# Optimization experiments

Measured on AMD Instinct MI355X. Metric: run time of the kernel, lower is better.

## Reference

```python
import jax, jax.numpy as jnp
import numpy as np

K = 8
LOCAL_WINDOW_RATIO = 0.25
NEG = -1e9
LN_EPS = 1e-5
NORM_EPS = 1e-12


def _window_indices(H, W):
    lws = max(3, int(min(H, W) * LOCAL_WINDOW_RATIO))
    if lws % 2 == 0:
        lws += 1
    half = lws // 2
    off = jnp.arange(-half, half + 1)
    dy, dx = jnp.meshgrid(off, off, indexing='ij')          # [lws,lws]
    dy = dy.reshape(-1); dx = dx.reshape(-1)                 # [w2]
    py, px = jnp.meshgrid(jnp.arange(H), jnp.arange(W), indexing='ij')
    py = py.reshape(-1); px = px.reshape(-1)                 # [HW]
    ny = py[:, None] + dy[None, :]                           # [HW,w2]
    nx = px[:, None] + dx[None, :]
    valid = (ny >= 0) & (ny < H) & (nx >= 0) & (nx < W)
    idx = jnp.clip(ny, 0, H - 1) * W + jnp.clip(nx, 0, W - 1)
    return idx, valid


def setup_inputs() -> dict:
    key = jax.random.key(0)
    ks = jax.random.split(key, 5)
    B, C, H, W = 4, 96, 48, 48
    return {
        'x': jax.random.normal(ks[0], (B, C, H, W), jnp.float32),
        'w1': jax.random.normal(ks[1], (2 * C, C), jnp.float32) * 0.05,
        'b1': jax.random.normal(ks[2], (2 * C,), jnp.float32) * 0.05,
        'w2': jax.random.normal(ks[3], (C, 2 * C), jnp.float32) * 0.05,
        'b2': jax.random.normal(ks[4], (C,), jnp.float32) * 0.05,
        'ln_w': jnp.ones((C,), jnp.float32),
        'ln_b': jnp.zeros((C,), jnp.float32),
    }


def reference(x, w1, b1, w2, b2, ln_w, ln_b):
    B, C, H, W = x.shape
    HW = H * W
    idx_w, valid = _window_indices(H, W)                     # [HW,w2]

    x_flat = x.transpose(0, 2, 3, 1).reshape(B, HW, C)       # [B,HW,C]
    n = jnp.linalg.norm(x_flat, axis=-1, keepdims=True)
    x_n = x_flat / jnp.maximum(n, NORM_EPS)

    win_n = x_n[:, idx_w, :]                                 # [B,HW,w2,C]
    sims = jnp.einsum('bpc,bpwc->bpw', x_n, win_n)           # cosine sim
    sims = jnp.where(valid[None], sims, NEG)

    # every pixel has >= (half+1)^2 >= K valid neighbors, so top-k stays valid
    top_sim, top_idx = jax.lax.top_k(sims, K)                # [B,HW,K]
    wts = jax.nn.softmax(top_sim, axis=-1)                   # exp/sum over top-k

    idx_g = jnp.take_along_axis(jnp.broadcast_to(idx_w[None], sims.shape), top_idx, axis=-1)  # [B,HW,K]
    feats = x_flat[jnp.arange(B)[:, None, None], idx_g]      # [B,HW,K,C] (un-normalized)
    agg = jnp.einsum('bpk,bpkc->bpc', wts, feats)            # [B,HW,C]

    mu = jnp.mean(x_flat, axis=-1, keepdims=True)
    var = jnp.var(x_flat, axis=-1, keepdims=True)
    x_ln = (x_flat - mu) / jnp.sqrt(var + LN_EPS) * ln_w + ln_b

    enhanced = agg + x_ln                                    # [B,HW,C]
    h = jax.nn.relu(jnp.einsum('bpc,dc->bpd', enhanced, w1) + b1)
    ffn = jnp.einsum('bpd,cd->bpc', h, w2) + b2
    out = enhanced + ffn
    return out.reshape(B, H, W, C).transpose(0, 3, 1, 2)
```

## Files before the change

### kernel.cpp

```cpp
#include <hip/hip_runtime.h>
#include <math.h>

#define BATCH 4
#define CH    96
#define HH    48
#define WW    48
#define HWPIX (HH*WW)
#define NPIX  (BATCH*HWPIX)
#define WIN   13
#define WIN2  169
#define HALF  6
#define TOPK  8
#define NEGV  (-1000000000.0f)

__global__ __launch_bounds__(256) void k0_wt(
    const float* __restrict__ w1, const float* __restrict__ w2,
    float* __restrict__ w1T, float* __restrict__ w2T)
{
    __shared__ float tile[32][33];
    int bid = blockIdx.x;
    const float* src; float* dst; int R, C, tr, tc;
    if (bid < 18) { src = w1; dst = w1T; R = 192; C = 96;  tr = bid / 3; tc = bid % 3; }
    else { int b2 = bid - 18; src = w2; dst = w2T; R = 96; C = 192; tr = b2 / 6; tc = b2 % 6; }
    int r0 = tr * 32, c0 = tc * 32;
    int tx = threadIdx.x & 31, ty = threadIdx.x >> 5;

    #pragma unroll
    for (int i = 0; i < 4; ++i) {
        int r = ty + i * 8;
        tile[r][tx] = src[(r0 + r) * C + c0 + tx];
    }
    __syncthreads();
    #pragma unroll
    for (int i = 0; i < 4; ++i) {
        int r = ty + i * 8;
        dst[(c0 + r) * R + r0 + tx] = tile[tx][r];
    }
}

__global__ __launch_bounds__(256) void k1_prep(
    const float* __restrict__ x, float* __restrict__ xt2,
    float* __restrict__ invn, float* __restrict__ muv, float* __restrict__ rsd)
{
    __shared__ float lds[96][33];
    int bid = blockIdx.x;
    int b   = bid / 72;
    int p0  = (bid % 72) * 32;
    int t   = threadIdx.x;

    #pragma unroll
    for (int it = 0; it < 12; ++it) {
        int e = t + it * 256;
        int c = e >> 5;
        int p = e & 31;
        lds[c][p] = x[(b * CH + c) * HWPIX + p0 + p];
    }
    __syncthreads();

    if (t < 32) {
        float s = 0.f, ss = 0.f;
        #pragma unroll
        for (int c = 0; c < CH; ++c) { float v = lds[c][t]; s += v; ss += v * v; }
        int gpix = b * HWPIX + p0 + t;
        invn[gpix] = 1.0f / fmaxf(sqrtf(ss), 1e-12f);
        float m = s * (1.0f / 96.0f);
        muv[gpix] = m;
        rsd[gpix] = rsqrtf(ss * (1.0f / 96.0f) - m * m + 1e-5f);
    }

    float4* x4 = (float4*)xt2;
    #pragma unroll
    for (int it = 0; it < 3; ++it) {
        int i = t + it * 256;
        int p = i & 31;
        int s = i >> 5;
        float4 v = make_float4(lds[4*s][p], lds[4*s+1][p],
                               lds[4*s+2][p], lds[4*s+3][p]);
        x4[s * NPIX + b * HWPIX + p0 + p] = v;
    }
}

__global__ __launch_bounds__(256) void k2_knn(
    const float* __restrict__ xt2, const float* __restrict__ invn,
    const float* __restrict__ muv, const float* __restrict__ rsd,
    const float* __restrict__ lnw, const float* __restrict__ lnb,
    float* __restrict__ enh)
{
    __shared__ float own[4][96];
    int t    = threadIdx.x;
    int wv   = t >> 6;
    int lane = t & 63;
    int gp   = blockIdx.x * 4 + wv;
    int b    = gp / HWPIX;
    int p    = gp - b * HWPIX;
    int py   = p / WW;
    int px   = p - py * WW;
    const float4* x4 = (const float4*)xt2;

    float4 ownv = make_float4(0.f, 0.f, 0.f, 0.f);
    if (lane < 24) {
        ownv = x4[lane * NPIX + gp];
        ((float4*)(own[wv]))[lane] = ownv;
    }
    float inp = invn[gp];
    float mu  = muv[gp];
    float rs  = rsd[gp];

    float v0 = -2e9f, v1 = -2e9f, v2 = -2e9f;
    const float4* ov = (const float4*)(own[wv]);
    #pragma unroll
    for (int k = 0; k < 3; ++k) {
        int n = lane + 64 * k;
        float sim = -2e9f;
        if (n < WIN2) {
            int dy = n / WIN - HALF;
            int dx = n - (dy + HALF) * WIN - HALF;
            int ny = py + dy, nx = px + dx;
            if (ny >= 0 && ny < HH && nx >= 0 && nx < WW) {
                int q = b * HWPIX + ny * WW + nx;
                float inq = invn[q];
                const float4* rp = x4 + q;
                float ax = 0.f, ay = 0.f, az = 0.f, aw = 0.f;
                #pragma unroll
                for (int s = 0; s < 24; ++s) {
                    float4 a  = ov[s];
                    float4 bb = rp[s * NPIX];
                    ax += a.x * bb.x; ay += a.y * bb.y;
                    az += a.z * bb.z; aw += a.w * bb.w;
                }
                sim = ((ax + ay) + (az + aw)) * inp * inq;
            } else {
                sim = NEGV;
            }
        }
        if (k == 0) v0 = sim; else if (k == 1) v1 = sim; else v2 = sim;
    }

    float tv[TOPK]; int tn[TOPK];
    #pragma unroll
    for (int r = 0; r < TOPK; ++r) {
        float m = fmaxf(fmaxf(v0, v1), v2);
        #pragma unroll
        for (int off = 1; off < 64; off <<= 1)
            m = fmaxf(m, __shfl_xor(m, off));
        unsigned long long m0 = __ballot(v0 == m);
        unsigned long long m1 = __ballot(v1 == m);
        unsigned long long m2 = __ballot(v2 == m);
        int n;
        if (m0)      n = (int)__builtin_ctzll(m0);
        else if (m1) n = 64 + (int)__builtin_ctzll(m1);
        else         n = 128 + (int)__builtin_ctzll(m2);
        tv[r] = m; tn[r] = n;
        int kk = n >> 6, ll = n & 63;
        if (ll == lane) {
            if (kk == 0)      v0 = -2e9f;
            else if (kk == 1) v1 = -2e9f;
            else              v2 = -2e9f;
        }
    }

    float wts[TOPK]; int qn[TOPK];
    float wsum = 0.f;
    #pragma unroll
    for (int r = 0; r < TOPK; ++r) {
        float e = expf(tv[r] - tv[0]);
        wts[r] = e; wsum += e;
        int n  = tn[r];
        int dy = n / WIN - HALF;
        int dx = n - (dy + HALF) * WIN - HALF;
        int gy = min(max(py + dy, 0), HH - 1);
        int gx = min(max(px + dx, 0), WW - 1);
        qn[r]  = b * HWPIX + gy * WW + gx;
    }
    float winv = 1.0f / wsum;

    if (lane < 24) {
        const float4* base = x4 + lane * NPIX;
        float4 g = make_float4(0.f, 0.f, 0.f, 0.f);
        #pragma unroll
        for (int r = 0; r < TOPK; ++r) {
            float4 f = base[qn[r]];
            float w = wts[r];
            g.x += w * f.x; g.y += w * f.y;
            g.z += w * f.z; g.w += w * f.w;
        }
        float4 lw = ((const float4*)lnw)[lane];
        float4 lb = ((const float4*)lnb)[lane];
        float4 e;
        e.x = g.x * winv + (ownv.x - mu) * rs * lw.x + lb.x;
        e.y = g.y * winv + (ownv.y - mu) * rs * lw.y + lb.y;
        e.z = g.z * winv + (ownv.z - mu) * rs * lw.z + lb.z;
        e.w = g.w * winv + (ownv.w - mu) * rs * lw.w + lb.w;
        ((float4*)(enh + gp * CH))[lane] = e;
    }
}

__global__ __launch_bounds__(384) void k3_ffn(
    const float* __restrict__ enh, const float* __restrict__ w1T,
    const float* __restrict__ b1, const float* __restrict__ w2T,
    const float* __restrict__ b2, float* __restrict__ out)
{
    __shared__ float el[8][100];
    __shared__ float hl[8][200];
    int g  = blockIdx.x;
    int b  = g / 288;
    int p0 = (g % 288) * 8;
    int t  = threadIdx.x;

    #pragma unroll
    for (int i = 0; i < 2; ++i) {
        int e = t + i * 384;
        int r = e / 96, c = e - r * 96;
        el[r][c] = enh[(b * HWPIX + p0 + r) * CH + c];
    }
    __syncthreads();

    {
        int j  = (t >= 192) ? t - 192 : t;
        int pg = (t >= 192) ? 1 : 0;
        const float4* e0 = (const float4*)(&el[pg    ][0]);
        const float4* e1 = (const float4*)(&el[pg + 2][0]);
        const float4* e2 = (const float4*)(&el[pg + 4][0]);
        const float4* e3 = (const float4*)(&el[pg + 6][0]);
        float a0 = 0.f, a1 = 0.f, a2 = 0.f, a3 = 0.f;
        #pragma unroll 6
        for (int c4 = 0; c4 < 24; ++c4) {
            float wa = w1T[(4*c4 + 0) * 192 + j];
            float wb = w1T[(4*c4 + 1) * 192 + j];
            float wc = w1T[(4*c4 + 2) * 192 + j];
            float wd = w1T[(4*c4 + 3) * 192 + j];
            float4 v0 = e0[c4], v1 = e1[c4], v2 = e2[c4], v3 = e3[c4];
            a0 += v0.x*wa + v0.y*wb + v0.z*wc + v0.w*wd;
            a1 += v1.x*wa + v1.y*wb + v1.z*wc + v1.w*wd;
            a2 += v2.x*wa + v2.y*wb + v2.z*wc + v2.w*wd;
            a3 += v3.x*wa + v3.y*wb + v3.z*wc + v3.w*wd;
        }
        float bj = b1[j];
        hl[pg    ][j] = fmaxf(a0 + bj, 0.f);
        hl[pg + 2][j] = fmaxf(a1 + bj, 0.f);
        hl[pg + 4][j] = fmaxf(a2 + bj, 0.f);
        hl[pg + 6][j] = fmaxf(a3 + bj, 0.f);
    }
    __syncthreads();

    {
        int c  = t % 96;
        int qg = t / 96;
        const float4* h0 = (const float4*)(&hl[qg    ][0]);
        const float4* h1 = (const float4*)(&hl[qg + 4][0]);
        float s0 = 0.f, s1 = 0.f;
        #pragma unroll 6
        for (int j4 = 0; j4 < 48; ++j4) {
            float wa = w2T[(4*j4 + 0) * 96 + c];
            float wb = w2T[(4*j4 + 1) * 96 + c];
            float wc = w2T[(4*j4 + 2) * 96 + c];
            float wd = w2T[(4*j4 + 3) * 96 + c];
            float4 u0 = h0[j4], u1 = h1[j4];
            s0 += u0.x*wa + u0.y*wb + u0.z*wc + u0.w*wd;
            s1 += u1.x*wa + u1.y*wb + u1.z*wc + u1.w*wd;
        }
        float bc = b2[c];
        out[(b * CH + c) * HWPIX + p0 + qg    ] = el[qg    ][c] + s0 + bc;
        out[(b * CH + c) * HWPIX + p0 + qg + 4] = el[qg + 4][c] + s1 + bc;
    }
}

extern "C" void kernel_launch(void* const* d_in, const int* in_sizes, int n_in,
                              void* d_out, int out_size, void* d_ws, size_t ws_size,
                              hipStream_t stream)
{
    const float* x   = (const float*)d_in[0];
    const float* w1  = (const float*)d_in[1];
    const float* b1  = (const float*)d_in[2];
    const float* w2  = (const float*)d_in[3];
    const float* b2  = (const float*)d_in[4];
    const float* lnw = (const float*)d_in[5];
    const float* lnb = (const float*)d_in[6];
    float* out = (float*)d_out;

    float* xt2 = out;

    float* ws   = (float*)d_ws;
    float* enh  = ws;
    float* invn = enh + NPIX * CH;
    float* muv  = invn + NPIX;
    float* rsd  = muv + NPIX;
    float* w1T  = rsd + NPIX;
    float* w2T  = w1T + 192 * 96;

    hipLaunchKernelGGL(k0_wt, dim3(36), dim3(256), 0, stream,
                       w1, w2, w1T, w2T);
    hipLaunchKernelGGL(k1_prep, dim3(288), dim3(256), 0, stream,
                       x, xt2, invn, muv, rsd);
    hipLaunchKernelGGL(k2_knn, dim3(NPIX / 4), dim3(256), 0, stream,
                       xt2, invn, muv, rsd, lnw, lnb, enh);
    hipLaunchKernelGGL(k3_ffn, dim3(1152), dim3(384), 0, stream,
                       enh, w1T, b1, w2T, b2, out);
}
```

Measured before the change: 85.13 us.

## Shrink FFN tile to four pixels and read activations directly from global memory

The FFN kernel now handles 4 pixels per block with 192 threads instead of 8 pixels with 384, and drops the shared-memory staging of the enhanced activations. Those activations are read straight from global memory, where all threads load the same addresses, and are reread for the residual add. The second matmul runs on only 96 of the 192 threads, each computing four outputs. This removes one barrier and some shared memory, but halves weight reuse per block, so w1T/w2T traffic doubles and half the threads sit idle in the second stage.

Measured after the change: 76.35 us. -10.3%, faster.

```diff
diff --git a/kernel.cpp b/kernel.cpp
--- a/kernel.cpp
+++ b/kernel.cpp
@@ -195,33 +195,23 @@
     }
 }
 
-__global__ __launch_bounds__(384) void k3_ffn(
+__global__ __launch_bounds__(192) void k3_ffn(
     const float* __restrict__ enh, const float* __restrict__ w1T,
     const float* __restrict__ b1, const float* __restrict__ w2T,
     const float* __restrict__ b2, float* __restrict__ out)
 {
-    __shared__ float el[8][100];
-    __shared__ float hl[8][200];
+    __shared__ float hl[4][200];
     int g  = blockIdx.x;
-    int b  = g / 288;
-    int p0 = (g % 288) * 8;
+    int b  = g / 576;
+    int p0 = (g % 576) * 4;
     int t  = threadIdx.x;
 
-    #pragma unroll
-    for (int i = 0; i < 2; ++i) {
-        int e = t + i * 384;
-        int r = e / 96, c = e - r * 96;
-        el[r][c] = enh[(b * HWPIX + p0 + r) * CH + c];
-    }
-    __syncthreads();
-
     {
-        int j  = (t >= 192) ? t - 192 : t;
-        int pg = (t >= 192) ? 1 : 0;
-        const float4* e0 = (const float4*)(&el[pg    ][0]);
-        const float4* e1 = (const float4*)(&el[pg + 2][0]);
-        const float4* e2 = (const float4*)(&el[pg + 4][0]);
-        const float4* e3 = (const float4*)(&el[pg + 6][0]);
+        int j = t;
+        const float4* e0 = (const float4*)(enh + (b * HWPIX + p0 + 0) * CH);
+        const float4* e1 = (const float4*)(enh + (b * HWPIX + p0 + 1) * CH);
+        const float4* e2 = (const float4*)(enh + (b * HWPIX + p0 + 2) * CH);
+        const float4* e3 = (const float4*)(enh + (b * HWPIX + p0 + 3) * CH);
         float a0 = 0.f, a1 = 0.f, a2 = 0.f, a3 = 0.f;
         #pragma unroll 6
         for (int c4 = 0; c4 < 24; ++c4) {
@@ -229,39 +219,51 @@
             float wb = w1T[(4*c4 + 1) * 192 + j];
             float wc = w1T[(4*c4 + 2) * 192 + j];
             float wd = w1T[(4*c4 + 3) * 192 + j];
-            float4 v0 = e0[c4], v1 = e1[c4], v2 = e2[c4], v3 = e3[c4];
+            float4 v0 = e0[c4];
+            float4 v1 = e1[c4];
+            float4 v2 = e2[c4];
+            float4 v3 = e3[c4];
             a0 += v0.x*wa + v0.y*wb + v0.z*wc + v0.w*wd;
             a1 += v1.x*wa + v1.y*wb + v1.z*wc + v1.w*wd;
             a2 += v2.x*wa + v2.y*wb + v2.z*wc + v2.w*wd;
             a3 += v3.x*wa + v3.y*wb + v3.z*wc + v3.w*wd;
         }
         float bj = b1[j];
-        hl[pg    ][j] = fmaxf(a0 + bj, 0.f);
-        hl[pg + 2][j] = fmaxf(a1 + bj, 0.f);
-        hl[pg + 4][j] = fmaxf(a2 + bj, 0.f);
-        hl[pg + 6][j] = fmaxf(a3 + bj, 0.f);
+        hl[0][j] = fmaxf(a0 + bj, 0.f);
+        hl[1][j] = fmaxf(a1 + bj, 0.f);
+        hl[2][j] = fmaxf(a2 + bj, 0.f);
+        hl[3][j] = fmaxf(a3 + bj, 0.f);
     }
     __syncthreads();
 
-    {
-        int c  = t % 96;
-        int qg = t / 96;
-        const float4* h0 = (const float4*)(&hl[qg    ][0]);
-        const float4* h1 = (const float4*)(&hl[qg + 4][0]);
-        float s0 = 0.f, s1 = 0.f;
+    if (t < 96) {
+        int c = t;
+        const float4* h0 = (const float4*)(&hl[0][0]);
+        const float4* h1 = (const float4*)(&hl[1][0]);
+        const float4* h2 = (const float4*)(&hl[2][0]);
+        const float4* h3 = (const float4*)(&hl[3][0]);
+        float s0 = 0.f, s1 = 0.f, s2 = 0.f, s3 = 0.f;
         #pragma unroll 6
         for (int j4 = 0; j4 < 48; ++j4) {
             float wa = w2T[(4*j4 + 0) * 96 + c];
             float wb = w2T[(4*j4 + 1) * 96 + c];
             float wc = w2T[(4*j4 + 2) * 96 + c];
             float wd = w2T[(4*j4 + 3) * 96 + c];
-            float4 u0 = h0[j4], u1 = h1[j4];
+            float4 u0 = h0[j4], u1 = h1[j4], u2 = h2[j4], u3 = h3[j4];
             s0 += u0.x*wa + u0.y*wb + u0.z*wc + u0.w*wd;
             s1 += u1.x*wa + u1.y*wb + u1.z*wc + u1.w*wd;
+            s2 += u2.x*wa + u2.y*wb + u2.z*wc + u2.w*wd;
+            s3 += u3.x*wa + u3.y*wb + u3.z*wc + u3.w*wd;
         }
         float bc = b2[c];
-        out[(b * CH + c) * HWPIX + p0 + qg    ] = el[qg    ][c] + s0 + bc;
-        out[(b * CH + c) * HWPIX + p0 + qg + 4] = el[qg + 4][c] + s1 + bc;
+        out[(b * CH + c) * HWPIX + p0 + 0] =
+            enh[(b * HWPIX + p0 + 0) * CH + c] + s0 + bc;
+        out[(b * CH + c) * HWPIX + p0 + 1] =
+            enh[(b * HWPIX + p0 + 1) * CH + c] + s1 + bc;
+        out[(b * CH + c) * HWPIX + p0 + 2] =
+            enh[(b * HWPIX + p0 + 2) * CH + c] + s2 + bc;
+        out[(b * CH + c) * HWPIX + p0 + 3] =
+            enh[(b * HWPIX + p0 + 3) * CH + c] + s3 + bc;
     }
 }
 
@@ -294,6 +296,6 @@
                        x, xt2, invn, muv, rsd);
     hipLaunchKernelGGL(k2_knn, dim3(NPIX / 4), dim3(256), 0, stream,
                        xt2, invn, muv, rsd, lnw, lnb, enh);
-    hipLaunchKernelGGL(k3_ffn, dim3(1152), dim3(384), 0, stream,
+    hipLaunchKernelGGL(k3_ffn, dim3(2304), dim3(192), 0, stream,
                        enh, w1T, b1, w2T, b2, out);
 }
```
